# Optimization experiments

Hardware: AMD Instinct MI355X
Metric: run time of the kernel (lower is better)

## Reference

```python
import jax, jax.numpy as jnp
import numpy as np

UNITS = 4096
INPUT_DIM = 1024
N = 16384


def setup_inputs() -> dict:
    key = jax.random.key(0)
    k1, k2 = jax.random.split(key)
    inputs = jax.random.normal(k1, (N, INPUT_DIM), dtype=jnp.float32)
    # Keras 'random_normal' initializer: stddev 0.05
    w = jax.random.normal(k2, (UNITS, INPUT_DIM), dtype=jnp.float32) * 0.05
    return {"inputs": inputs, "w": w}


def reference(inputs, w):
    # Pairwise squared Euclidean distance: out[n, u] = sum_d (w[u,d] - x[n,d])^2
    x_sq = jnp.sum(inputs * inputs, axis=-1, keepdims=True)        # [N, 1]
    w_sq = jnp.sum(w * w, axis=-1)                                  # [U]
    cross = jnp.einsum("nd,ud->nu", inputs, w)                     # [N, U]
    return x_sq + w_sq[None, :] - 2.0 * cross
```

## Files before the change

### kernel.cpp

```cpp
#include <hip/hip_runtime.h>
#include <cstdint>
#include <cstddef>

#define AS1 __attribute__((address_space(1)))
#define AS3 __attribute__((address_space(3)))

typedef unsigned int u32;
typedef unsigned char u8;
typedef int i32x4 __attribute__((ext_vector_type(4)));
typedef int i32x8 __attribute__((ext_vector_type(8)));
typedef float f32x4 __attribute__((ext_vector_type(4)));

constexpr int D  = 1024;
constexpr int NS = 16384;
constexpr int US = 4096;
constexpr int BM = 256, BN = 256, BK = 128;
constexpr int KT = D / BK;

constexpr size_t XQ_OFF  = 0;
constexpr size_t WQ_OFF  = (size_t)NS * D;
constexpr size_t XSQ_OFF = WQ_OFF + (size_t)US * D;
constexpr size_t WSQ_OFF = XSQ_OFF + (size_t)NS * 4;

__global__ __launch_bounds__(256) void quant_sq(
    const float* __restrict__ x, const float* __restrict__ w,
    u8* __restrict__ xq, u8* __restrict__ wq,
    float* __restrict__ xsq, float* __restrict__ wsq) {
  const int lane = threadIdx.x & 63;
  const int wave = blockIdx.x * 4 + (threadIdx.x >> 6);
  const int nwaves = gridDim.x * 4;
  for (int row = wave; row < NS + US; row += nwaves) {
    const float* src; u8* qdst; float* sdst; int r; float qscale;
    if (row < NS) { src = x; qdst = xq; sdst = xsq; r = row; qscale = 1.0f; }
    else          { src = w; qdst = wq; sdst = wsq; r = row - NS; qscale = 16.0f; }
    const float4* s4 = (const float4*)(src + (size_t)r * D);
    u32* qrow = (u32*)(qdst + (size_t)r * D);
    float s = 0.f;
#pragma unroll
    for (int it = 0; it < 4; ++it) {
      const float4 v = s4[it * 64 + lane];
      s += v.x * v.x + v.y * v.y + v.z * v.z + v.w * v.w;
      u32 p01 = __builtin_amdgcn_cvt_pk_fp8_f32(v.x * qscale, v.y * qscale, 0, false);
      u32 w0  = __builtin_amdgcn_cvt_pk_fp8_f32(v.z * qscale, v.w * qscale, p01, true);
      qrow[it * 64 + lane] = w0;
    }
#pragma unroll
    for (int off = 32; off; off >>= 1) s += __shfl_down(s, off, 64);
    if (lane == 0) sdst[r] = s;
  }
}

__global__ __launch_bounds__(512, 2) void dist_gemm(
    const u8* __restrict__ xq, const u8* __restrict__ wq,
    const float* __restrict__ xsq, const float* __restrict__ wsq,
    float* __restrict__ out) {
  __shared__ u8 lds[2 * 65536];

  const int tid = threadIdx.x;
  const int lane = tid & 63;
  const int wv = tid >> 6;
  const int wm = wv >> 2;
  const int wn = wv & 3;
  const int quad = lane >> 4;
  const int l15 = lane & 15;

  const int m0 = blockIdx.y * BM;
  const int n0 = blockIdx.x * BN;

  const int srow = tid >> 3;
  const int sch = lane & 7;

  f32x4 acc[8][4];
#pragma unroll
  for (int mt = 0; mt < 8; ++mt)
#pragma unroll
    for (int nt = 0; nt < 4; ++nt) acc[mt][nt] = (f32x4){0.f, 0.f, 0.f, 0.f};

  auto stageA = [&](int buf, int kt, int sw) {
    const int r = sw * 64 + srow;
    const int cg = sch ^ (r & 7);
    const u8* g = xq + (size_t)(m0 + r) * D + kt * BK + cg * 16;
    __builtin_amdgcn_global_load_lds((AS1 void*)(u8*)g,
        (AS3 void*)(lds + buf * 65536 + sw * 8192 + wv * 1024), 16, 0, 0);
  };
  auto stageB = [&](int buf, int kt, int sw) {
    const int r = sw * 64 + srow;
    const int cg = sch ^ (r & 7);
    const u8* g = wq + (size_t)(n0 + r) * D + kt * BK + cg * 16;
    __builtin_amdgcn_global_load_lds((AS1 void*)(u8*)g,
        (AS3 void*)(lds + buf * 65536 + 32768 + sw * 8192 + wv * 1024), 16, 0, 0);
  };
  auto ldfrag = [&](const u8* mat, int row) -> i32x8 {
    const int s = row & 7;
    const i32x4 f0 = *reinterpret_cast<const i32x4*>(mat + row * BK + ((2 * quad) ^ s) * 16);
    const i32x4 f1 = *reinterpret_cast<const i32x4*>(mat + row * BK + ((2 * quad + 1) ^ s) * 16);
    return __builtin_shufflevector(f0, f1, 0, 1, 2, 3, 4, 5, 6, 7);
  };

  stageA(0, 0, 0); stageA(0, 0, 2);
#pragma unroll
  for (int sw = 0; sw < 4; ++sw) stageB(0, 0, sw);
  stageA(0, 0, 1); stageA(0, 0, 3);
#pragma unroll
  for (int sw = 0; sw < 4; ++sw) stageA(1, 1, sw);
#pragma unroll
  for (int sw = 0; sw < 4; ++sw) stageB(1, 1, sw);
  asm volatile("s_waitcnt vmcnt(10)" ::: "memory");
  __builtin_amdgcn_sched_barrier(0);
  __builtin_amdgcn_s_barrier();
  __builtin_amdgcn_sched_barrier(0);

#define MM(MT, NT, AF) \
  acc[MT][NT] = __builtin_amdgcn_mfma_scale_f32_16x16x128_f8f6f4( \
      AF, bf[NT], acc[MT][NT], 0, 0, 0, 0x7F7F7F7F, 0, 0x7F7F7F7F)

#define OPEN_PHASE() do { \
    __builtin_amdgcn_sched_barrier(0); \
    __builtin_amdgcn_s_barrier(); \
    asm volatile("s_waitcnt lgkmcnt(0)" ::: "memory"); \
    __builtin_amdgcn_sched_barrier(0); \
    __builtin_amdgcn_s_setprio(1); } while (0)

#define CLOSE_PHASE() do { \
    __builtin_amdgcn_s_setprio(0); \
    __builtin_amdgcn_sched_barrier(0); \
    __builtin_amdgcn_s_barrier(); \
    __builtin_amdgcn_sched_barrier(0); } while (0)

#pragma unroll
  for (int t = 0; t < KT - 1; ++t) {
    const u8* sA = lds + (t & 1) * 65536;
    const u8* sB = sA + 32768;
    const int nb = (t + 1) & 1;
    const int ar = wm * 128 + l15;
    const int br = wn * 64 + l15;

    i32x8 bf[4];

    {
      bf[0] = ldfrag(sB, br);
      bf[1] = ldfrag(sB, br + 16);
      bf[2] = ldfrag(sB, br + 32);
      bf[3] = ldfrag(sB, br + 48);
      i32x8 a0 = ldfrag(sA, ar);
      i32x8 a1 = ldfrag(sA, ar + 16);
      if (t >= 1) { stageA(nb, t + 1, 1); stageA(nb, t + 1, 3); }
      OPEN_PHASE();
      MM(0, 0, a0); MM(0, 1, a0); MM(0, 2, a0); MM(0, 3, a0);
      MM(1, 0, a1); MM(1, 1, a1); MM(1, 2, a1); MM(1, 3, a1);
      CLOSE_PHASE();
    }
    {
      i32x8 a0 = ldfrag(sA, ar + 32);
      i32x8 a1 = ldfrag(sA, ar + 48);
      if (t + 2 < KT) { stageB(t & 1, t + 2, 0); stageB(t & 1, t + 2, 1); stageB(t & 1, t + 2, 2); }
      OPEN_PHASE();
      MM(2, 0, a0); MM(2, 1, a0); MM(2, 2, a0); MM(2, 3, a0);
      MM(3, 0, a1); MM(3, 1, a1); MM(3, 2, a1); MM(3, 3, a1);
      CLOSE_PHASE();
    }
    {
      if (t == 0) {
        asm volatile("s_waitcnt vmcnt(11)" ::: "memory");
        __builtin_amdgcn_sched_barrier(0);
      }
      i32x8 a0 = ldfrag(sA, ar + 64);
      i32x8 a1 = ldfrag(sA, ar + 80);
      if (t + 2 < KT) { stageB(t & 1, t + 2, 3); stageA(t & 1, t + 2, 0); stageA(t & 1, t + 2, 2); }
      OPEN_PHASE();
      MM(4, 0, a0); MM(4, 1, a0); MM(4, 2, a0); MM(4, 3, a0);
      MM(5, 0, a1); MM(5, 1, a1); MM(5, 2, a1); MM(5, 3, a1);
      CLOSE_PHASE();
    }
    {
      i32x8 a0 = ldfrag(sA, ar + 96);
      i32x8 a1 = ldfrag(sA, ar + 112);
      OPEN_PHASE();
      MM(6, 0, a0); MM(6, 1, a0); MM(6, 2, a0); MM(6, 3, a0);
      MM(7, 0, a1); MM(7, 1, a1); MM(7, 2, a1); MM(7, 3, a1);
      __builtin_amdgcn_s_setprio(0);
      __builtin_amdgcn_sched_barrier(0);
      if (t + 2 < KT) asm volatile("s_waitcnt vmcnt(6)" ::: "memory");
      else            asm volatile("s_waitcnt vmcnt(0)" ::: "memory");
      __builtin_amdgcn_sched_barrier(0);
      __builtin_amdgcn_s_barrier();
      __builtin_amdgcn_sched_barrier(0);
    }
  }

  {
    const u8* sA = lds + 65536;
    const u8* sB = sA + 32768;
    const int ar = wm * 128 + l15;
    const int br = wn * 64 + l15;

    float wsv[4];
#pragma unroll
    for (int nt = 0; nt < 4; ++nt) wsv[nt] = wsq[n0 + wn * 64 + nt * 16 + l15];

    i32x8 bf[4];
    bf[0] = ldfrag(sB, br);
    bf[1] = ldfrag(sB, br + 16);
    bf[2] = ldfrag(sB, br + 32);
    bf[3] = ldfrag(sB, br + 48);

    auto xs_of = [&](int mt) -> f32x4 {
      return *reinterpret_cast<const f32x4*>(xsq + m0 + wm * 128 + mt * 16 + quad * 4);
    };
    auto store2 = [&](int mt, const f32x4 xs) {
      const int R0 = m0 + wm * 128 + mt * 16 + quad * 4;
#pragma unroll
      for (int nt = 0; nt < 4; ++nt) {
        const int C = n0 + wn * 64 + nt * 16 + l15;
#pragma unroll
        for (int r = 0; r < 4; ++r)
          out[(size_t)(R0 + r) * US + C] = xs[r] + wsv[nt] - 0.125f * acc[mt][nt][r];
      }
    };

    f32x4 xs0 = xs_of(0), xs1 = xs_of(1);
    {
      i32x8 a0 = ldfrag(sA, ar);
      i32x8 a1 = ldfrag(sA, ar + 16);
      __builtin_amdgcn_s_setprio(1);
      MM(0, 0, a0); MM(0, 1, a0); MM(0, 2, a0); MM(0, 3, a0);
      MM(1, 0, a1); MM(1, 1, a1); MM(1, 2, a1); MM(1, 3, a1);
      __builtin_amdgcn_s_setprio(0);
    }
    f32x4 xs2 = xs_of(2), xs3 = xs_of(3);
    {
      i32x8 a0 = ldfrag(sA, ar + 32);
      i32x8 a1 = ldfrag(sA, ar + 48);
      __builtin_amdgcn_s_setprio(1);
      MM(2, 0, a0); MM(2, 1, a0); MM(2, 2, a0); MM(2, 3, a0);
      MM(3, 0, a1); MM(3, 1, a1); MM(3, 2, a1); MM(3, 3, a1);
      __builtin_amdgcn_s_setprio(0);
    }
    store2(0, xs0); store2(1, xs1);
    f32x4 xs4 = xs_of(4), xs5 = xs_of(5);
    {
      i32x8 a0 = ldfrag(sA, ar + 64);
      i32x8 a1 = ldfrag(sA, ar + 80);
      __builtin_amdgcn_s_setprio(1);
      MM(4, 0, a0); MM(4, 1, a0); MM(4, 2, a0); MM(4, 3, a0);
      MM(5, 0, a1); MM(5, 1, a1); MM(5, 2, a1); MM(5, 3, a1);
      __builtin_amdgcn_s_setprio(0);
    }
    store2(2, xs2); store2(3, xs3);
    f32x4 xs6 = xs_of(6), xs7 = xs_of(7);
    {
      i32x8 a0 = ldfrag(sA, ar + 96);
      i32x8 a1 = ldfrag(sA, ar + 112);
      __builtin_amdgcn_s_setprio(1);
      MM(6, 0, a0); MM(6, 1, a0); MM(6, 2, a0); MM(6, 3, a0);
      MM(7, 0, a1); MM(7, 1, a1); MM(7, 2, a1); MM(7, 3, a1);
      __builtin_amdgcn_s_setprio(0);
    }
    store2(4, xs4); store2(5, xs5);
    store2(6, xs6); store2(7, xs7);
  }
}

extern "C" void kernel_launch(void* const* d_in, const int* in_sizes, int n_in,
                              void* d_out, int out_size, void* d_ws, size_t ws_size,
                              hipStream_t stream) {
  const float* x = (const float*)d_in[0];
  const float* w = (const float*)d_in[1];
  float* out = (float*)d_out;
  char* ws = (char*)d_ws;

  u8* xq = (u8*)(ws + XQ_OFF);
  u8* wq = (u8*)(ws + WQ_OFF);
  float* xsq = (float*)(ws + XSQ_OFF);
  float* wsq = (float*)(ws + WSQ_OFF);

  quant_sq<<<dim3(1280), dim3(256), 0, stream>>>(x, w, xq, wq, xsq, wsq);
  dist_gemm<<<dim3(US / BN, NS / BM), dim3(512), 0, stream>>>(xq, wq, xsq, wsq, out);
}
```

Measured before the change: 376.9 us.

## Software-pipeline LDS fragment loads one MFMA phase ahead within the K loop

Restructures the main K loop so the A fragments for the next MFMA phase are read from LDS while the current phase's MFMAs run. The first A fragments of the next tile are prefetched at the end of each iteration and carried into the tail. The goal is to hide LDS read latency behind matrix-core work, at the cost of more live vector registers. Barrier placement and vmcnt wait counts are changed to match, which risks races if the counts are wrong.

```diff
diff --git a/kernel.cpp b/kernel.cpp
--- a/kernel.cpp
+++ b/kernel.cpp
@@ -97,102 +97,110 @@
     return __builtin_shufflevector(f0, f1, 0, 1, 2, 3, 4, 5, 6, 7);
   };
 
-  stageA(0, 0, 0); stageA(0, 0, 2);
+  const int ar = wm * 128 + l15;
+  const int br = wn * 64 + l15;
+
+#pragma unroll
+  for (int sw = 0; sw < 4; ++sw) stageA(0, 0, sw);
 #pragma unroll
   for (int sw = 0; sw < 4; ++sw) stageB(0, 0, sw);
-  stageA(0, 0, 1); stageA(0, 0, 3);
 #pragma unroll
   for (int sw = 0; sw < 4; ++sw) stageA(1, 1, sw);
 #pragma unroll
   for (int sw = 0; sw < 4; ++sw) stageB(1, 1, sw);
-  asm volatile("s_waitcnt vmcnt(10)" ::: "memory");
-  __builtin_amdgcn_sched_barrier(0);
-  __builtin_amdgcn_s_barrier();
+  asm volatile("s_waitcnt vmcnt(8)" ::: "memory");
   __builtin_amdgcn_sched_barrier(0);
 
 #define MM(MT, NT, AF) \
   acc[MT][NT] = __builtin_amdgcn_mfma_scale_f32_16x16x128_f8f6f4( \
       AF, bf[NT], acc[MT][NT], 0, 0, 0, 0x7F7F7F7F, 0, 0x7F7F7F7F)
 
-#define OPEN_PHASE() do { \
-    __builtin_amdgcn_sched_barrier(0); \
-    __builtin_amdgcn_s_barrier(); \
-    asm volatile("s_waitcnt lgkmcnt(0)" ::: "memory"); \
-    __builtin_amdgcn_sched_barrier(0); \
-    __builtin_amdgcn_s_setprio(1); } while (0)
-
-#define CLOSE_PHASE() do { \
-    __builtin_amdgcn_s_setprio(0); \
-    __builtin_amdgcn_sched_barrier(0); \
-    __builtin_amdgcn_s_barrier(); \
-    __builtin_amdgcn_sched_barrier(0); } while (0)
+#define SB() __builtin_amdgcn_sched_barrier(0)
+
+  i32x8 a00, a01;
 
 #pragma unroll
   for (int t = 0; t < KT - 1; ++t) {
     const u8* sA = lds + (t & 1) * 65536;
     const u8* sB = sA + 32768;
     const int nb = (t + 1) & 1;
-    const int ar = wm * 128 + l15;
-    const int br = wn * 64 + l15;
+    const u8* nA = lds + nb * 65536;
+    const int cur = t & 1;
 
     i32x8 bf[4];
 
-    {
-      bf[0] = ldfrag(sB, br);
-      bf[1] = ldfrag(sB, br + 16);
-      bf[2] = ldfrag(sB, br + 32);
-      bf[3] = ldfrag(sB, br + 48);
-      i32x8 a0 = ldfrag(sA, ar);
-      i32x8 a1 = ldfrag(sA, ar + 16);
-      if (t >= 1) { stageA(nb, t + 1, 1); stageA(nb, t + 1, 3); }
-      OPEN_PHASE();
-      MM(0, 0, a0); MM(0, 1, a0); MM(0, 2, a0); MM(0, 3, a0);
-      MM(1, 0, a1); MM(1, 1, a1); MM(1, 2, a1); MM(1, 3, a1);
-      CLOSE_PHASE();
-    }
-    {
-      i32x8 a0 = ldfrag(sA, ar + 32);
-      i32x8 a1 = ldfrag(sA, ar + 48);
-      if (t + 2 < KT) { stageB(t & 1, t + 2, 0); stageB(t & 1, t + 2, 1); stageB(t & 1, t + 2, 2); }
-      OPEN_PHASE();
-      MM(2, 0, a0); MM(2, 1, a0); MM(2, 2, a0); MM(2, 3, a0);
-      MM(3, 0, a1); MM(3, 1, a1); MM(3, 2, a1); MM(3, 3, a1);
-      CLOSE_PHASE();
-    }
-    {
-      if (t == 0) {
-        asm volatile("s_waitcnt vmcnt(11)" ::: "memory");
-        __builtin_amdgcn_sched_barrier(0);
-      }
-      i32x8 a0 = ldfrag(sA, ar + 64);
-      i32x8 a1 = ldfrag(sA, ar + 80);
-      if (t + 2 < KT) { stageB(t & 1, t + 2, 3); stageA(t & 1, t + 2, 0); stageA(t & 1, t + 2, 2); }
-      OPEN_PHASE();
-      MM(4, 0, a0); MM(4, 1, a0); MM(4, 2, a0); MM(4, 3, a0);
-      MM(5, 0, a1); MM(5, 1, a1); MM(5, 2, a1); MM(5, 3, a1);
-      CLOSE_PHASE();
-    }
-    {
-      i32x8 a0 = ldfrag(sA, ar + 96);
-      i32x8 a1 = ldfrag(sA, ar + 112);
-      OPEN_PHASE();
-      MM(6, 0, a0); MM(6, 1, a0); MM(6, 2, a0); MM(6, 3, a0);
-      MM(7, 0, a1); MM(7, 1, a1); MM(7, 2, a1); MM(7, 3, a1);
-      __builtin_amdgcn_s_setprio(0);
-      __builtin_amdgcn_sched_barrier(0);
-      if (t + 2 < KT) asm volatile("s_waitcnt vmcnt(6)" ::: "memory");
-      else            asm volatile("s_waitcnt vmcnt(0)" ::: "memory");
-      __builtin_amdgcn_sched_barrier(0);
-      __builtin_amdgcn_s_barrier();
-      __builtin_amdgcn_sched_barrier(0);
-    }
+    __builtin_amdgcn_s_barrier();
+    SB();
+    bf[0] = ldfrag(sB, br);
+    bf[1] = ldfrag(sB, br + 16);
+    bf[2] = ldfrag(sB, br + 32);
+    bf[3] = ldfrag(sB, br + 48);
+    if (t == 0) { a00 = ldfrag(sA, ar); a01 = ldfrag(sA, ar + 16); }
+    asm volatile("s_waitcnt lgkmcnt(0)" ::: "memory");
+    SB();
+    __builtin_amdgcn_s_setprio(1);
+    if (t >= 1) { stageA(nb, t + 1, 1); stageA(nb, t + 1, 3); }
+    i32x8 a02 = ldfrag(sA, ar + 32);
+    i32x8 a03 = ldfrag(sA, ar + 48);
+    SB();
+    MM(0, 0, a00); MM(0, 1, a00); MM(0, 2, a00); MM(0, 3, a00);
+    MM(1, 0, a01); MM(1, 1, a01); MM(1, 2, a01); MM(1, 3, a01);
+    __builtin_amdgcn_s_setprio(0);
+    SB();
+
+    __builtin_amdgcn_s_barrier();
+    SB();
+    asm volatile("s_waitcnt lgkmcnt(0)" ::: "memory");
+    SB();
+    __builtin_amdgcn_s_setprio(1);
+    if (t + 2 < KT) { stageB(cur, t + 2, 0); stageB(cur, t + 2, 1); stageB(cur, t + 2, 2); }
+    i32x8 a04 = ldfrag(sA, ar + 64);
+    i32x8 a05 = ldfrag(sA, ar + 80);
+    SB();
+    MM(2, 0, a02); MM(2, 1, a02); MM(2, 2, a02); MM(2, 3, a02);
+    MM(3, 0, a03); MM(3, 1, a03); MM(3, 2, a03); MM(3, 3, a03);
+    __builtin_amdgcn_s_setprio(0);
+    SB();
+
+    __builtin_amdgcn_s_barrier();
+    SB();
+    asm volatile("s_waitcnt lgkmcnt(0)" ::: "memory");
+    SB();
+    __builtin_amdgcn_s_setprio(1);
+    if (t + 2 < KT) { stageB(cur, t + 2, 3); stageA(cur, t + 2, 0); stageA(cur, t + 2, 2); }
+    i32x8 a06 = ldfrag(sA, ar + 96);
+    i32x8 a07 = ldfrag(sA, ar + 112);
+    SB();
+    MM(4, 0, a04); MM(4, 1, a04); MM(4, 2, a04); MM(4, 3, a04);
+    MM(5, 0, a05); MM(5, 1, a05); MM(5, 2, a05); MM(5, 3, a05);
+    __builtin_amdgcn_s_setprio(0);
+    SB();
+    if (t < KT - 2) asm volatile("s_waitcnt vmcnt(6)" ::: "memory");
+    else            asm volatile("s_waitcnt vmcnt(2)" ::: "memory");
+    SB();
+
+    __builtin_amdgcn_s_barrier();
+    SB();
+    asm volatile("s_waitcnt lgkmcnt(0)" ::: "memory");
+    SB();
+    __builtin_amdgcn_s_setprio(1);
+    a00 = ldfrag(nA, ar);
+    a01 = ldfrag(nA, ar + 16);
+    SB();
+    MM(6, 0, a06); MM(6, 1, a06); MM(6, 2, a06); MM(6, 3, a06);
+    MM(7, 0, a07); MM(7, 1, a07); MM(7, 2, a07); MM(7, 3, a07);
+    __builtin_amdgcn_s_setprio(0);
+    SB();
   }
+
+  asm volatile("s_waitcnt vmcnt(0)" ::: "memory");
+  SB();
+  __builtin_amdgcn_s_barrier();
+  SB();
 
   {
     const u8* sA = lds + 65536;
     const u8* sB = sA + 32768;
-    const int ar = wm * 128 + l15;
-    const int br = wn * 64 + l15;
 
     float wsv[4];
 #pragma unroll
@@ -220,11 +228,9 @@
 
     f32x4 xs0 = xs_of(0), xs1 = xs_of(1);
     {
-      i32x8 a0 = ldfrag(sA, ar);
-      i32x8 a1 = ldfrag(sA, ar + 16);
-      __builtin_amdgcn_s_setprio(1);
-      MM(0, 0, a0); MM(0, 1, a0); MM(0, 2, a0); MM(0, 3, a0);
-      MM(1, 0, a1); MM(1, 1, a1); MM(1, 2, a1); MM(1, 3, a1);
+      __builtin_amdgcn_s_setprio(1);
+      MM(0, 0, a00); MM(0, 1, a00); MM(0, 2, a00); MM(0, 3, a00);
+      MM(1, 0, a01); MM(1, 1, a01); MM(1, 2, a01); MM(1, 3, a01);
       __builtin_amdgcn_s_setprio(0);
     }
     f32x4 xs2 = xs_of(2), xs3 = xs_of(3);
```

New measurement: 379.0 us. Within noise of the previous version (+0.6%).
